# Performance work log

Hardware: AMD Instinct MI355X
Metric: run time of the kernel (lower is better)

## Reference

```python
import jax, jax.numpy as jnp
import numpy as np

B, C, H, W = 8, 512, 64, 64
IC = C // 2  # inter_channel


def setup_inputs() -> dict:
    key = jax.random.key(0)
    ks = jax.random.split(key, 10)
    s = 0.02
    return {
        "x": jax.random.normal(ks[0], (B, C, H, W), dtype=jnp.float32),
        "y": jax.random.normal(ks[1], (B, C, H, W), dtype=jnp.float32),
        "w_phi": jax.random.normal(ks[2], (IC, C), dtype=jnp.float32) * s,
        "b_phi": jnp.zeros((IC,), dtype=jnp.float32),
        "w_theta": jax.random.normal(ks[3], (IC, C), dtype=jnp.float32) * s,
        "b_theta": jnp.zeros((IC,), dtype=jnp.float32),
        "w_g": jax.random.normal(ks[4], (IC, C), dtype=jnp.float32) * s,
        "b_g": jnp.zeros((IC,), dtype=jnp.float32),
        "w_mask": jax.random.normal(ks[5], (C, IC), dtype=jnp.float32) * s,
        "b_mask": jnp.zeros((C,), dtype=jnp.float32),
    }


def _conv1x1(w, b, t):
    # t: [b, cin, h, w]; 1x1 conv == channel matmul
    return jnp.einsum('oc,bchw->bohw', w, t) + b[None, :, None, None]


def reference(x, y, w_phi, b_phi, w_theta, b_theta, w_g, b_g, w_mask, b_mask):
    b, c, h, w = x.shape
    ic = w_phi.shape[0]  # c // 2
    # Faithful to the torch code: conv outputs ic channels but is viewed as
    # (b, c, -1), so the sequence length is N = h*w//2 and feature dim is c.
    x_phi = _conv1x1(w_phi, b_phi, y).reshape(b, c, -1)              # [b, c, N]
    x_theta = _conv1x1(w_theta, b_theta, x).reshape(b, c, -1)
    x_theta = jnp.transpose(x_theta, (0, 2, 1))                      # [b, N, c]
    x_g = _conv1x1(w_g, b_g, x).reshape(b, c, -1)
    dict
    x_g = jnp.transpose(x_g, (0, 2, 1))                              # [b, N, c]
    scores = jnp.einsum('bnc,bcm->bnm', x_theta, x_phi)              # [b, N, N]
    attn = jax.nn.softmax(scores, axis=1)  # softmax over dim=1 (columns), as in torch
    out_nl = jnp.einsum('bnm,bmc->bnc', attn, x_g)                   # [b, N, c]
    out_nl = jnp.transpose(out_nl, (0, 2, 1)).reshape(b, ic, h, w)   # [b, ic, h, w]
    mask = _conv1x1(w_mask, b_mask, out_nl)                          # [b, c, h, w]
    return mask + x
```

## Files before the change

### kernel.cpp

```cpp
#include <hip/hip_runtime.h>
#include <hip/hip_bf16.h>


typedef __attribute__((ext_vector_type(8))) short short8;
typedef __attribute__((ext_vector_type(4))) short short4v;
typedef __attribute__((ext_vector_type(4))) float f32x4;

__device__ __forceinline__ short f2bf(float f) {
  union { __hip_bfloat16 h; short s; } u; u.h = __float2bfloat16(f); return u.s;
}
__device__ __forceinline__ float bf2f(short s) {
  union { short s; __hip_bfloat16 h; } u; u.s = s; return __bfloat162float(u.h);
}

__device__ __forceinline__ void async_ld16(const void* g, void* l) {
  __builtin_amdgcn_global_load_lds(
      (const __attribute__((address_space(1))) unsigned int*)(unsigned long long)g,
      (__attribute__((address_space(3))) unsigned int*)(unsigned int)(unsigned long long)l,
      16, 0, 0);
}

__device__ __forceinline__ short8 frag_sw(const short* Ds, int row, int q8)
{
  return *(const short8*)&Ds[row * 32 + (((q8 >> 3) ^ ((row >> 2) & 3)) << 3)];
}

__global__ __launch_bounds__(512, 4)
void ov_k(const short* __restrict__ Eg, const short* __restrict__ Gg,
          short* __restrict__ Cg)
{
  const int L = blockIdx.x;
  const int xcd = L & 7, k = L >> 3;
  const int slab = xcd + ((k >> 2) << 3);
  const int bz = slab >> 4, by = slab & 15, bx = k & 3;

  __shared__ __align__(16) short As[2][128 * 32];
  __shared__ __align__(16) short Bs[2][128 * 32];
  const short* A = Eg + ((long)bz << 22);
  const short* B = Gg + ((long)bz << 20);
  const int m0 = by * 128;
  const int n0 = bx * 128;
  const int t = threadIdx.x;
  const int wv = t >> 6, ln = t & 63;
  const int wr = wv >> 1, wc = wv & 1;
  const int fr = ln & 15, q8 = (ln >> 4) * 8;
  const int rowA = t >> 2;
  const int kcs = ((t & 3) ^ ((t >> 4) & 3)) * 8;

  f32x4 acc[2][4];
  #pragma unroll
  for (int i = 0; i < 2; i++)
    #pragma unroll
    for (int j = 0; j < 4; j++)
      #pragma unroll
      for (int r = 0; r < 4; r++) acc[i][j][r] = 0.f;

  async_ld16(A + (long)(m0 + rowA) * 2048 + kcs, &As[0][0] + wv * 512);
  async_ld16(B + (long)(n0 + rowA) * 2048 + kcs, &Bs[0][0] + wv * 512);
  __syncthreads();

  for (int kt = 1; kt < 64; kt++) {
    const int cur = (kt - 1) & 1, nxt = kt & 1;
    async_ld16(A + (long)(m0 + rowA) * 2048 + kt * 32 + kcs, &As[nxt][0] + wv * 512);
    async_ld16(B + (long)(n0 + rowA) * 2048 + kt * 32 + kcs, &Bs[nxt][0] + wv * 512);
    short8 af[2], bfr[4];
    #pragma unroll
    for (int mi = 0; mi < 2; mi++) af[mi] = frag_sw(&As[cur][0], wr * 32 + mi * 16 + fr, q8);
    #pragma unroll
    for (int ni = 0; ni < 4; ni++) bfr[ni] = frag_sw(&Bs[cur][0], wc * 64 + ni * 16 + fr, q8);
    #pragma unroll
    for (int mi = 0; mi < 2; mi++)
      #pragma unroll
      for (int ni = 0; ni < 4; ni++)
        acc[mi][ni] = __builtin_amdgcn_mfma_f32_16x16x32_bf16(af[mi], bfr[ni], acc[mi][ni], 0, 0, 0);
    __syncthreads();
  }
  {
    short8 af[2], bfr[4];
    #pragma unroll
    for (int mi = 0; mi < 2; mi++) af[mi] = frag_sw(&As[1][0], wr * 32 + mi * 16 + fr, q8);
    #pragma unroll
    for (int ni = 0; ni < 4; ni++) bfr[ni] = frag_sw(&Bs[1][0], wc * 64 + ni * 16 + fr, q8);
    #pragma unroll
    for (int mi = 0; mi < 2; mi++)
      #pragma unroll
      for (int ni = 0; ni < 4; ni++)
        acc[mi][ni] = __builtin_amdgcn_mfma_f32_16x16x32_bf16(af[mi], bfr[ni], acc[mi][ni], 0, 0, 0);
  }

  const int colb = n0 + wc * 64 + fr;
  const int rowb = m0 + wr * 32 + (ln >> 4) * 4;
  #pragma unroll
  for (int mi = 0; mi < 2; mi++)
    #pragma unroll
    for (int r = 0; r < 4; r++) {
      const int mr = rowb + mi * 16 + r;
      #pragma unroll
      for (int ni = 0; ni < 4; ni++)
        Cg[((long)bz << 20) + (long)mr * 512 + colb + ni * 16] = f2bf(acc[mi][ni][r]);
    }
}

__global__ __launch_bounds__(512, 2)
void conv_ptg(const float* __restrict__ x, const float* __restrict__ y,
              const short* __restrict__ wth, const short* __restrict__ wph,
              const short* __restrict__ wg,
              const float* __restrict__ bth, const float* __restrict__ bph,
              const float* __restrict__ bg,
              short* __restrict__ TPT2, short* __restrict__ G)
{
  __shared__ __align__(16) short As[2][128 * 32];
  __shared__ __align__(16) short Bs[2][256 * 32];
  __shared__ __align__(16) short Cs[2][256 * 32];
  const int slab = blockIdx.x;
  const bool isphi = slab >= 256;
  const bool doG = !isphi;
  const int s2 = slab & 255;
  const int img = s2 >> 5;
  const float* src = (isphi ? y : x) + (long)img * (512L * 4096);
  const int px0 = (s2 & 31) * 128;
  const long m0 = (long)slab * 128;
  const short* W = isphi ? wph : wth;
  const float* bias = isphi ? bph : bth;
  const int t = threadIdx.x;
  const int wv = t >> 6, ln = t & 63;
  const int wpx = wv >> 2, wic = wv & 3;
  const int fr = ln & 15, q8 = (ln >> 4) * 8;
  const int g4 = (t >> 5) * 4, p4 = (t & 31) * 4;
  const int w2 = wv - 4;
  const int kcs = ((ln & 3) ^ (ln >> 4)) * 8;

  f32x4 acc[4][4], accg[4][4];
  #pragma unroll
  for (int i = 0; i < 4; i++)
    #pragma unroll
    for (int j = 0; j < 4; j++)
      #pragma unroll
      for (int r = 0; r < 4; r++) { acc[i][j][r] = 0.f; accg[i][j][r] = 0.f; }

  if (t >= 256) {
    #pragma unroll
    for (int j = 0; j < 4; j++)
      async_ld16(W + (long)(w2 * 64 + j * 16 + (ln >> 2)) * 512 + kcs,
                 &Bs[0][(w2 * 64 + j * 16) * 32]);
    if (doG) {
      #pragma unroll
      for (int j = 0; j < 4; j++)
        async_ld16(wg + (long)(w2 * 64 + j * 16 + (ln >> 2)) * 512 + kcs,
                   &Cs[0][(w2 * 64 + j * 16) * 32]);
    }
  } else {
    f32x4 r[4];
    #pragma unroll
    for (int i = 0; i < 4; i++)
      r[i] = *(const f32x4*)&src[(long)(g4 + i) * 4096 + px0 + p4];
    #pragma unroll
    for (int j = 0; j < 4; j++) {
      short4v w;
      w[0] = f2bf(r[0][j]); w[1] = f2bf(r[1][j]); w[2] = f2bf(r[2][j]); w[3] = f2bf(r[3][j]);
      const int px = p4 + j;
      const int u = (g4 >> 3) ^ ((px >> 2) & 3);
      *(short4v*)&As[0][px * 32 + u * 8 + (g4 & 4)] = w;
    }
  }
  __syncthreads();

  for (int k = 1; k < 16; k++) {
    const int cur = (k - 1) & 1, nxt = k & 1;
    f32x4 r[4];
    if (t >= 256) {
      #pragma unroll
      for (int j = 0; j < 4; j++)
        async_ld16(W + (long)(w2 * 64 + j * 16 + (ln >> 2)) * 512 + k * 32 + kcs,
                   &Bs[nxt][(w2 * 64 + j * 16) * 32]);
      if (doG) {
        #pragma unroll
        for (int j = 0; j < 4; j++)
          async_ld16(wg + (long)(w2 * 64 + j * 16 + (ln >> 2)) * 512 + k * 32 + kcs,
                     &Cs[nxt][(w2 * 64 + j * 16) * 32]);
      }
    } else {
      #pragma unroll
      for (int i = 0; i < 4; i++)
        r[i] = *(const f32x4*)&src[(long)(k * 32 + g4 + i) * 4096 + px0 + p4];
    }
    short8 af[4], bfv[4];
    #pragma unroll
    for (int mi = 0; mi < 4; mi++) af[mi] = frag_sw(&As[cur][0], wpx * 64 + mi * 16 + fr, q8);
    #pragma unroll
    for (int ni = 0; ni < 4; ni++) bfv[ni] = frag_sw(&Bs[cur][0], wic * 64 + ni * 16 + fr, q8);
    #pragma unroll
    for (int mi = 0; mi < 4; mi++)
      #pragma unroll
      for (int ni = 0; ni < 4; ni++)
        acc[mi][ni] = __builtin_amdgcn_mfma_f32_16x16x32_bf16(af[mi], bfv[ni], acc[mi][ni], 0, 0, 0);
    if (doG) {
      short8 ag[4], bg2[4];
      #pragma unroll
      for (int mi = 0; mi < 4; mi++) ag[mi] = frag_sw(&Cs[cur][0], wic * 64 + mi * 16 + fr, q8);
      #pragma unroll
      for (int ni = 0; ni < 4; ni++) bg2[ni] = frag_sw(&As[cur][0], wpx * 64 + ni * 16 + fr, q8);
      #pragma unroll
      for (int mi = 0; mi < 4; mi++)
        #pragma unroll
        for (int ni = 0; ni < 4; ni++)
          accg[mi][ni] = __builtin_amdgcn_mfma_f32_16x16x32_bf16(ag[mi], bg2[ni], accg[mi][ni], 0, 0, 0);
    }
    if (t < 256) {
      #pragma unroll
      for (int j = 0; j < 4; j++) {
        short4v w;
        w[0] = f2bf(r[0][j]); w[1] = f2bf(r[1][j]); w[2] = f2bf(r[2][j]); w[3] = f2bf(r[3][j]);
        const int px = p4 + j;
        const int u = (g4 >> 3) ^ ((px >> 2) & 3);
        *(short4v*)&As[nxt][px * 32 + u * 8 + (g4 & 4)] = w;
      }
    }
    __syncthreads();
  }

  {
    short8 af[4], bfv[4];
    #pragma unroll
    for (int mi = 0; mi < 4; mi++) af[mi] = frag_sw(&As[1][0], wpx * 64 + mi * 16 + fr, q8);
    #pragma unroll
    for (int ni = 0; ni < 4; ni++) bfv[ni] = frag_sw(&Bs[1][0], wic * 64 + ni * 16 + fr, q8);
    #pragma unroll
    for (int mi = 0; mi < 4; mi++)
      #pragma unroll
      for (int ni = 0; ni < 4; ni++)
        acc[mi][ni] = __builtin_amdgcn_mfma_f32_16x16x32_bf16(af[mi], bfv[ni], acc[mi][ni], 0, 0, 0);
    if (doG) {
      short8 ag[4], bg2[4];
      #pragma unroll
      for (int mi = 0; mi < 4; mi++) ag[mi] = frag_sw(&Cs[1][0], wic * 64 + mi * 16 + fr, q8);
      #pragma unroll
      for (int ni = 0; ni < 4; ni++) bg2[ni] = frag_sw(&As[1][0], wpx * 64 + ni * 16 + fr, q8);
      #pragma unroll
      for (int mi = 0; mi < 4; mi++)
        #pragma unroll
        for (int ni = 0; ni < 4; ni++)
          accg[mi][ni] = __builtin_amdgcn_mfma_f32_16x16x32_bf16(ag[mi], bg2[ni], accg[mi][ni], 0, 0, 0);
    }
  }

  const int colic = wic * 64 + fr;
  float cb[4];
  #pragma unroll
  for (int ni = 0; ni < 4; ni++) cb[ni] = bias[colic + ni * 16];
  #pragma unroll
  for (int mi = 0; mi < 4; mi++)
    #pragma unroll
    for (int r = 0; r < 4; r++) {
      const long m = m0 + wpx * 64 + mi * 16 + (ln >> 4) * 4 + r;
      #pragma unroll
      for (int ni = 0; ni < 4; ni++)
        TPT2[m * 256 + colic + ni * 16] = f2bf(acc[mi][ni][r] + cb[ni]);
    }

  if (doG) {
    const int colpx = px0 + wpx * 64 + fr;
    #pragma unroll
    for (int mi = 0; mi < 4; mi++)
      #pragma unroll
      for (int r = 0; r < 4; r++) {
        const int ic = wic * 64 + mi * 16 + (ln >> 4) * 4 + r;
        const float badd = bg[ic];
        #pragma unroll
        for (int ni = 0; ni < 4; ni++)
          G[((long)img << 20) + (long)ic * 4096 + colpx + ni * 16] = f2bf(accg[mi][ni][r] + badd);
      }
  }
}

__global__ __launch_bounds__(256)
void scores_k(const short* __restrict__ TT2, const short* __restrict__ PT2,
              short* __restrict__ ST, float* __restrict__ pstats)
{
  __shared__ __align__(16) short As[2][128 * 32];
  __shared__ __align__(16) short Bs[2][128 * 32];
  const int bz = blockIdx.z, by = blockIdx.y, bx = blockIdx.x;
  const int t = threadIdx.x;
  const int wv = t >> 6, ln = t & 63;
  const int wm = (wv >> 1) * 64, wn = (wv & 1) * 64;
  const int fr = ln & 15, q8 = (ln >> 4) * 8;
  const int rowA = t >> 2;
  const int kcs = ((t & 3) ^ ((t >> 4) & 3)) * 8;

  const short* Abase = TT2 + ((long)(bz * 4096 + by * 128)) * 256;
  const short* Bbase = PT2 + ((long)(bz * 4096 + bx * 128)) * 256;

  f32x4 acc[4][4];
  #pragma unroll
  for (int i = 0; i < 4; i++)
    #pragma unroll
    for (int j = 0; j < 4; j++)
      #pragma unroll
      for (int r = 0; r < 4; r++) acc[i][j][r] = 0.f;

  #define SC_STAGE(s, buf)                                                     \
    {                                                                          \
      const long hoff = (long)((s) >> 3) * 2048 * 256;                         \
      const int kk = ((s) & 7) * 32;                                           \
      _Pragma("unroll")                                                        \
      for (int sv = 0; sv < 2; sv++) {                                         \
        async_ld16(Abase + hoff + (long)(sv * 64 + rowA) * 256 + kk + kcs,     \
                   &As[buf][0] + (sv * 256 + wv * 64) * 8);                    \
        async_ld16(Bbase + hoff + (long)(sv * 64 + rowA) * 256 + kk + kcs,     \
                   &Bs[buf][0] + (sv * 256 + wv * 64) * 8);                    \
      }                                                                        \
    }

  SC_STAGE(0, 0);
  __syncthreads();
  for (int s = 1; s < 16; s++) {
    const int cur = (s - 1) & 1, nxt = s & 1;
    SC_STAGE(s, nxt);
    short8 af[4], bfr[4];
    #pragma unroll
    for (int mi = 0; mi < 4; mi++) af[mi] = frag_sw(&As[cur][0], wm + mi * 16 + fr, q8);
    #pragma unroll
    for (int ni = 0; ni < 4; ni++) bfr[ni] = frag_sw(&Bs[cur][0], wn + ni * 16 + fr, q8);
    #pragma unroll
    for (int mi = 0; mi < 4; mi++)
      #pragma unroll
      for (int ni = 0; ni < 4; ni++)
        acc[mi][ni] = __builtin_amdgcn_mfma_f32_16x16x32_bf16(af[mi], bfr[ni], acc[mi][ni], 0, 0, 0);
    __syncthreads();
  }
  {
    short8 af[4], bfr[4];
    #pragma unroll
    for (int mi = 0; mi < 4; mi++) af[mi] = frag_sw(&As[1][0], wm + mi * 16 + fr, q8);
    #pragma unroll
    for (int ni = 0; ni < 4; ni++) bfr[ni] = frag_sw(&Bs[1][0], wn + ni * 16 + fr, q8);
    #pragma unroll
    for (int mi = 0; mi < 4; mi++)
      #pragma unroll
      for (int ni = 0; ni < 4; ni++)
        acc[mi][ni] = __builtin_amdgcn_mfma_f32_16x16x32_bf16(af[mi], bfr[ni], acc[mi][ni], 0, 0, 0);
  }
  #undef SC_STAGE

  const int colb = bx * 128 + wn + fr;
  const int rowb = by * 128 + wm + (ln >> 4) * 4;
  short* base = ST + ((long)bz << 22);
  float ps[4] = {0.f, 0.f, 0.f, 0.f};
  #pragma unroll
  for (int mi = 0; mi < 4; mi++)
    #pragma unroll
    for (int r = 0; r < 4; r++) {
      const long mr = rowb + mi * 16 + r;
      #pragma unroll
      for (int ni = 0; ni < 4; ni++) {
        float e = __expf(acc[mi][ni][r]);
        base[mr * 2048 + colb + ni * 16] = f2bf(e);
        ps[ni] += e;
      }
    }
  #pragma unroll
  for (int ni = 0; ni < 4; ni++) {
    ps[ni] += __shfl_xor(ps[ni], 16);
    ps[ni] += __shfl_xor(ps[ni], 32);
  }
  float* part = (float*)&As[0][0];
  if (ln < 16) {
    #pragma unroll
    for (int ni = 0; ni < 4; ni++)
      part[(wv >> 1) * 128 + wn + ni * 16 + fr] = ps[ni];
  }
  __syncthreads();
  if (t < 128)
    pstats[((long)(bz * 16 + by)) * 2048 + bx * 128 + t] = part[t] + part[128 + t];
}

__global__ __launch_bounds__(256)
void zfinal(const float* __restrict__ pstats, float* __restrict__ invZ)
{
  const int g = blockIdx.x * 256 + threadIdx.x;
  const int b = g >> 11, col = g & 2047;
  float S = 0.f;
  #pragma unroll
  for (int rc = 0; rc < 16; rc++) S += pstats[((long)(b * 16 + rc)) * 2048 + col];
  invZ[g] = 1.f / S;
}

__global__ __launch_bounds__(256)
void g_scale(short* __restrict__ G, const float* __restrict__ invZ)
{
  const long base = ((long)blockIdx.x * 256 + threadIdx.x) * 8;
  const int bz = (int)(base >> 20);
  const int n2 = (int)(base & 4095);
  const float* z = invZ + bz * 2048 + (n2 & 2047);
  short8 v = *(short8*)&G[base];
  f32x4 z0 = *(const f32x4*)z;
  f32x4 z1 = *(const f32x4*)(z + 4);
  #pragma unroll
  for (int j = 0; j < 4; j++) { v[j] = f2bf(bf2f(v[j]) * z0[j]); v[4 + j] = f2bf(bf2f(v[4 + j]) * z1[j]); }
  *(short8*)&G[base] = v;
}

__global__ __launch_bounds__(256)
void mask_k(const short* __restrict__ Wm20, const short* __restrict__ Wm21,
            const short* __restrict__ OVT, const float* __restrict__ bmask,
            const float* __restrict__ x, float* __restrict__ out)
{
  __shared__ __align__(16) short As[2][128 * 32];
  __shared__ __align__(16) short Bs[2][128 * 32];
  const int bz = blockIdx.z;
  const int n0 = blockIdx.x * 128;
  const int m0 = blockIdx.y * 128;
  const short* A = (n0 >= 2048) ? Wm21 : Wm20;
  const short* B = OVT + ((long)bz << 20) + (long)(n0 & 2047) * 512;
  const int t = threadIdx.x;
  const int wv = t >> 6, ln = t & 63;
  const int wm = (wv >> 1) * 64, wn = (wv & 1) * 64;
  const int fr = ln & 15, q8 = (ln >> 4) * 8;
  const int rowA = t >> 2;
  const int kcs = ((t & 3) ^ ((t >> 4) & 3)) * 8;

  f32x4 acc[4][4];
  #pragma unroll
  for (int i = 0; i < 4; i++)
    #pragma unroll
    for (int j = 0; j < 4; j++)
      #pragma unroll
      for (int r = 0; r < 4; r++) acc[i][j][r] = 0.f;

  #define MK_STAGE(s, buf)                                                     \
    {                                                                          \
      const int kk = (s) * 32;                                                 \
      _Pragma("unroll")                                                        \
      for (int sv = 0; sv < 2; sv++) {                                         \
        async_ld16(A + (long)(m0 + sv * 64 + rowA) * 512 + kk + kcs,           \
                   &As[buf][0] + (sv * 256 + wv * 64) * 8);                    \
        async_ld16(B + (long)(sv * 64 + rowA) * 512 + kk + kcs,                \
                   &Bs[buf][0] + (sv * 256 + wv * 64) * 8);                    \
      }                                                                        \
    }

  MK_STAGE(0, 0);
  __syncthreads();
  for (int s = 1; s < 16; s++) {
    const int cur = (s - 1) & 1, nxt = s & 1;
    MK_STAGE(s, nxt);
    short8 af[4], bfr[4];
    #pragma unroll
    for (int mi = 0; mi < 4; mi++) af[mi] = frag_sw(&As[cur][0], wm + mi * 16 + fr, q8);
    #pragma unroll
    for (int ni = 0; ni < 4; ni++) bfr[ni] = frag_sw(&Bs[cur][0], wn + ni * 16 + fr, q8);
    #pragma unroll
    for (int mi = 0; mi < 4; mi++)
      #pragma unroll
      for (int ni = 0; ni < 4; ni++)
        acc[mi][ni] = __builtin_amdgcn_mfma_f32_16x16x32_bf16(af[mi], bfr[ni], acc[mi][ni], 0, 0, 0);
    __syncthreads();
  }
  {
    short8 af[4], bfr[4];
    #pragma unroll
    for (int mi = 0; mi < 4; mi++) af[mi] = frag_sw(&As[1][0], wm + mi * 16 + fr, q8);
    #pragma unroll
    for (int ni = 0; ni < 4; ni++) bfr[ni] = frag_sw(&Bs[1][0], wn + ni * 16 + fr, q8);
    #pragma unroll
    for (int mi = 0; mi < 4; mi++)
      #pragma unroll
      for (int ni = 0; ni < 4; ni++)
        acc[mi][ni] = __builtin_amdgcn_mfma_f32_16x16x32_bf16(af[mi], bfr[ni], acc[mi][ni], 0, 0, 0);
  }
  #undef MK_STAGE

  const int colb = n0 + wn + fr;
  const int rowb = m0 + wm + (ln >> 4) * 4;
  #pragma unroll
  for (int mi = 0; mi < 4; mi++)
    #pragma unroll
    for (int r = 0; r < 4; r++) {
      const int mr = rowb + mi * 16 + r;
      const float badd = bmask[mr];
      const long rbase = ((long)bz * 512 + mr) * 4096;
      #pragma unroll
      for (int ni = 0; ni < 4; ni++) {
        const int cc = colb + ni * 16;
        out[rbase + cc] = acc[mi][ni][r] + badd + x[rbase + cc];
      }
    }
}

__global__ __launch_bounds__(256)
void wconv2(const float* w_phi, const float* w_theta, const float* w_g,
            const float* w_mask,
            short* wph, short* wth, short* wg, short* Wm20, short* Wm21)
{
  const int seg = blockIdx.x >> 6;
  const int blk = blockIdx.x & 63;
  const int i0 = blk * 2048 + threadIdx.x * 8;
  if (seg < 3) {
    const float* s = seg == 0 ? w_phi : seg == 1 ? w_theta : w_g;
    short* d = seg == 0 ? wph : seg == 1 ? wth : wg;
    f32x4 a = *(const f32x4*)&s[i0];
    f32x4 b = *(const f32x4*)&s[i0 + 4];
    short8 o;
    #pragma unroll
    for (int j = 0; j < 4; j++) { o[j] = f2bf(a[j]); o[4 + j] = f2bf(b[j]); }
    *(short8*)&d[i0] = o;
  } else {
    const int o = i0 >> 8;
    f32x4 a = *(const f32x4*)&w_mask[i0];
    f32x4 b = *(const f32x4*)&w_mask[i0 + 4];
    short v[8];
    #pragma unroll
    for (int j = 0; j < 4; j++) { v[j] = f2bf(a[j]); v[4 + j] = f2bf(b[j]); }
    short8 a0, a1, b0, b1;
    #pragma unroll
    for (int j = 0; j < 4; j++) {
      a0[2 * j] = v[j];     a0[2 * j + 1] = 0;
      a1[2 * j] = v[4 + j]; a1[2 * j + 1] = 0;
      b0[2 * j] = 0;        b0[2 * j + 1] = v[j];
      b1[2 * j] = 0;        b1[2 * j + 1] = v[4 + j];
    }
    const long base = (long)o * 512 + 2 * (i0 & 255);
    *(short8*)&Wm20[base] = a0; *(short8*)&Wm20[base + 8] = a1;
    *(short8*)&Wm21[base] = b0; *(short8*)&Wm21[base + 8] = b1;
  }
}

extern "C" void kernel_launch(void* const* d_in, const int* in_sizes, int n_in,
                              void* d_out, int out_size, void* d_ws, size_t ws_size,
                              hipStream_t stream)
{
  (void)in_sizes; (void)n_in; (void)out_size; (void)ws_size;
  const float* x       = (const float*)d_in[0];
  const float* y       = (const float*)d_in[1];
  const float* w_phi   = (const float*)d_in[2];
  const float* b_phi   = (const float*)d_in[3];
  const float* w_theta = (const float*)d_in[4];
  const float* b_theta = (const float*)d_in[5];
  const float* w_g     = (const float*)d_in[6];
  const float* b_g     = (const float*)d_in[7];
  const float* w_mask  = (const float*)d_in[8];
  const float* b_mask  = (const float*)d_in[9];
  float* out = (float*)d_out;

  char* ws = (char*)d_ws;
  const long MB = 1L << 20;
  short* wph  = (short*)(ws + 0);
  short* wth  = (short*)(ws + 256 * 1024);
  short* wg   = (short*)(ws + 512 * 1024);
  short* Wm20 = (short*)(ws + 768 * 1024);
  short* Wm21 = (short*)(ws + 1280 * 1024);
  short* TPT2 = (short*)(ws + 66 * MB);
  short* G    = (short*)(ws + 98 * MB);
  short* ST   = (short*)(ws + 2 * MB);
  float* pstats = (float*)(ws + 114 * MB);
  float* invZ   = (float*)(ws + 115 * MB);
  short* OVT  = (short*)(ws + 66 * MB);

  dim3 blk(256, 1, 1);
  dim3 blk8(512, 1, 1);

  wconv2<<<dim3(256, 1, 1), blk, 0, stream>>>(w_phi, w_theta, w_g, w_mask,
                                              wph, wth, wg, Wm20, Wm21);

  conv_ptg<<<dim3(512, 1, 1), blk8, 0, stream>>>(x, y, wth, wph, wg,
                                                 b_theta, b_phi, b_g, TPT2, G);

  scores_k<<<dim3(16, 16, 8), blk, 0, stream>>>(TPT2, TPT2 + 32768L * 256, ST, pstats);
  zfinal<<<dim3(64, 1, 1), blk, 0, stream>>>(pstats, invZ);
  g_scale<<<dim3(4096, 1, 1), blk, 0, stream>>>(G, invZ);

  ov_k<<<dim3(512, 1, 1), blk8, 0, stream>>>(ST, G, OVT);

  mask_k<<<dim3(32, 4, 8), blk, 0, stream>>>(Wm20, Wm21, OVT, b_mask, x, out);
}
```

Measured before the change: 372.3 us.

## Triple-buffer LDS in GEMM kernels with partial vmcnt waits

Converts the double-buffered async global-to-LDS pipelines in ov_k, scores_k and mask_k into three-stage pipelines. Each barrier now waits only until the previous stage's loads are done (vmcnt(N)), leaving one prefetch in flight. The goal is to hide global load latency behind MFMA work. LDS per block grows by half, which may limit occupancy, especially for ov_k with launch_bounds(512,4). The scores_k partial-stats scratch moves to buffer 1 to avoid clobbering data still in use.

```diff
diff --git a/kernel.cpp b/kernel.cpp
--- a/kernel.cpp
+++ b/kernel.cpp
@@ -20,6 +20,10 @@
       16, 0, 0);
 }
 
+#define CBAR(N)                                                                \
+  asm volatile("s_waitcnt vmcnt(" #N ") lgkmcnt(0)" ::: "memory");             \
+  __builtin_amdgcn_s_barrier();
+
 __device__ __forceinline__ short8 frag_sw(const short* Ds, int row, int q8)
 {
   return *(const short8*)&Ds[row * 32 + (((q8 >> 3) ^ ((row >> 2) & 3)) << 3)];
@@ -34,8 +38,8 @@
   const int slab = xcd + ((k >> 2) << 3);
   const int bz = slab >> 4, by = slab & 15, bx = k & 3;
 
-  __shared__ __align__(16) short As[2][128 * 32];
-  __shared__ __align__(16) short Bs[2][128 * 32];
+  __shared__ __align__(16) short As[3][128 * 32];
+  __shared__ __align__(16) short Bs[3][128 * 32];
   const short* A = Eg + ((long)bz << 22);
   const short* B = Gg + ((long)bz << 20);
   const int m0 = by * 128;
@@ -55,38 +59,48 @@
       #pragma unroll
       for (int r = 0; r < 4; r++) acc[i][j][r] = 0.f;
 
-  async_ld16(A + (long)(m0 + rowA) * 2048 + kcs, &As[0][0] + wv * 512);
-  async_ld16(B + (long)(n0 + rowA) * 2048 + kcs, &Bs[0][0] + wv * 512);
-  __syncthreads();
-
-  for (int kt = 1; kt < 64; kt++) {
-    const int cur = (kt - 1) & 1, nxt = kt & 1;
-    async_ld16(A + (long)(m0 + rowA) * 2048 + kt * 32 + kcs, &As[nxt][0] + wv * 512);
-    async_ld16(B + (long)(n0 + rowA) * 2048 + kt * 32 + kcs, &Bs[nxt][0] + wv * 512);
-    short8 af[2], bfr[4];
-    #pragma unroll
-    for (int mi = 0; mi < 2; mi++) af[mi] = frag_sw(&As[cur][0], wr * 32 + mi * 16 + fr, q8);
-    #pragma unroll
-    for (int ni = 0; ni < 4; ni++) bfr[ni] = frag_sw(&Bs[cur][0], wc * 64 + ni * 16 + fr, q8);
-    #pragma unroll
-    for (int mi = 0; mi < 2; mi++)
-      #pragma unroll
-      for (int ni = 0; ni < 4; ni++)
-        acc[mi][ni] = __builtin_amdgcn_mfma_f32_16x16x32_bf16(af[mi], bfr[ni], acc[mi][ni], 0, 0, 0);
-    __syncthreads();
-  }
-  {
-    short8 af[2], bfr[4];
-    #pragma unroll
-    for (int mi = 0; mi < 2; mi++) af[mi] = frag_sw(&As[1][0], wr * 32 + mi * 16 + fr, q8);
-    #pragma unroll
-    for (int ni = 0; ni < 4; ni++) bfr[ni] = frag_sw(&Bs[1][0], wc * 64 + ni * 16 + fr, q8);
-    #pragma unroll
-    for (int mi = 0; mi < 2; mi++)
-      #pragma unroll
-      for (int ni = 0; ni < 4; ni++)
-        acc[mi][ni] = __builtin_amdgcn_mfma_f32_16x16x32_bf16(af[mi], bfr[ni], acc[mi][ni], 0, 0, 0);
-  }
+  #define OV_STAGE(kt, buf)                                                    \
+    async_ld16(A + (long)(m0 + rowA) * 2048 + (kt) * 32 + kcs,                 \
+               &As[buf][0] + wv * 512);                                        \
+    async_ld16(B + (long)(n0 + rowA) * 2048 + (kt) * 32 + kcs,                 \
+               &Bs[buf][0] + wv * 512);
+
+  #define OV_COMPUTE(cbuf)                                                     \
+    {                                                                          \
+      const short* Ac = &As[cbuf][0];                                          \
+      const short* Bc = &Bs[cbuf][0];                                          \
+      short8 af[2], bfr[4];                                                    \
+      _Pragma("unroll")                                                        \
+      for (int mi = 0; mi < 2; mi++)                                           \
+        af[mi] = frag_sw(Ac, wr * 32 + mi * 16 + fr, q8);                      \
+      _Pragma("unroll")                                                        \
+      for (int ni = 0; ni < 4; ni++)                                           \
+        bfr[ni] = frag_sw(Bc, wc * 64 + ni * 16 + fr, q8);                     \
+      _Pragma("unroll")                                                        \
+      for (int mi = 0; mi < 2; mi++)                                           \
+        _Pragma("unroll")                                                      \
+        for (int ni = 0; ni < 4; ni++)                                         \
+          acc[mi][ni] = __builtin_amdgcn_mfma_f32_16x16x32_bf16(               \
+              af[mi], bfr[ni], acc[mi][ni], 0, 0, 0);                          \
+    }
+
+  OV_STAGE(0, 0);
+  OV_STAGE(1, 1);
+  CBAR(2)
+
+  int cs = 0, ss = 2;
+  for (int kt = 0; kt < 62; kt++) {
+    OV_STAGE(kt + 2, ss);
+    OV_COMPUTE(cs);
+    CBAR(2)
+    cs = (cs == 2) ? 0 : cs + 1;
+    ss = (ss == 2) ? 0 : ss + 1;
+  }
+  OV_COMPUTE(2)
+  CBAR(0)
+  OV_COMPUTE(0)
+  #undef OV_STAGE
+  #undef OV_COMPUTE
 
   const int colb = n0 + wc * 64 + fr;
   const int rowb = m0 + wr * 32 + (ln >> 4) * 4;
@@ -277,8 +291,8 @@
 void scores_k(const short* __restrict__ TT2, const short* __restrict__ PT2,
               short* __restrict__ ST, float* __restrict__ pstats)
 {
-  __shared__ __align__(16) short As[2][128 * 32];
-  __shared__ __align__(16) short Bs[2][128 * 32];
+  __shared__ __align__(16) short As[3][128 * 32];
+  __shared__ __align__(16) short Bs[3][128 * 32];
   const int bz = blockIdx.z, by = blockIdx.y, bx = blockIdx.x;
   const int t = threadIdx.x;
   const int wv = t >> 6, ln = t & 63;
@@ -311,36 +325,40 @@
       }                                                                        \
     }
 
+  #define SC_COMPUTE(cbuf)                                                     \
+    {                                                                          \
+      const short* Ac = &As[cbuf][0];                                          \
+      const short* Bc = &Bs[cbuf][0];                                          \
+      short8 af[4], bfr[4];                                                    \
+      _Pragma("unroll")                                                        \
+      for (int mi = 0; mi < 4; mi++) af[mi] = frag_sw(Ac, wm + mi * 16 + fr, q8); \
+      _Pragma("unroll")                                                        \
+      for (int ni = 0; ni < 4; ni++) bfr[ni] = frag_sw(Bc, wn + ni * 16 + fr, q8); \
+      _Pragma("unroll")                                                        \
+      for (int mi = 0; mi < 4; mi++)                                           \
+        _Pragma("unroll")                                                      \
+        for (int ni = 0; ni < 4; ni++)                                         \
+          acc[mi][ni] = __builtin_amdgcn_mfma_f32_16x16x32_bf16(               \
+              af[mi], bfr[ni], acc[mi][ni], 0, 0, 0);                          \
+    }
+
   SC_STAGE(0, 0);
-  __syncthreads();
-  for (int s = 1; s < 16; s++) {
-    const int cur = (s - 1) & 1, nxt = s & 1;
-    SC_STAGE(s, nxt);
-    short8 af[4], bfr[4];
-    #pragma unroll
-    for (int mi = 0; mi < 4; mi++) af[mi] = frag_sw(&As[cur][0], wm + mi * 16 + fr, q8);
-    #pragma unroll
-    for (int ni = 0; ni < 4; ni++) bfr[ni] = frag_sw(&Bs[cur][0], wn + ni * 16 + fr, q8);
-    #pragma unroll
-    for (int mi = 0; mi < 4; mi++)
-      #pragma unroll
-      for (int ni = 0; ni < 4; ni++)
-        acc[mi][ni] = __builtin_amdgcn_mfma_f32_16x16x32_bf16(af[mi], bfr[ni], acc[mi][ni], 0, 0, 0);
-    __syncthreads();
-  }
-  {
-    short8 af[4], bfr[4];
-    #pragma unroll
-    for (int mi = 0; mi < 4; mi++) af[mi] = frag_sw(&As[1][0], wm + mi * 16 + fr, q8);
-    #pragma unroll
-    for (int ni = 0; ni < 4; ni++) bfr[ni] = frag_sw(&Bs[1][0], wn + ni * 16 + fr, q8);
-    #pragma unroll
-    for (int mi = 0; mi < 4; mi++)
-      #pragma unroll
-      for (int ni = 0; ni < 4; ni++)
-        acc[mi][ni] = __builtin_amdgcn_mfma_f32_16x16x32_bf16(af[mi], bfr[ni], acc[mi][ni], 0, 0, 0);
-  }
+  SC_STAGE(1, 1);
+  CBAR(4)
+
+  int cs = 0, ss = 2;
+  for (int s = 0; s < 14; s++) {
+    SC_STAGE(s + 2, ss);
+    SC_COMPUTE(cs);
+    CBAR(4)
+    cs = (cs == 2) ? 0 : cs + 1;
+    ss = (ss == 2) ? 0 : ss + 1;
+  }
+  SC_COMPUTE(2)
+  CBAR(0)
+  SC_COMPUTE(0)
   #undef SC_STAGE
+  #undef SC_COMPUTE
 
   const int colb = bx * 128 + wn + fr;
   const int rowb = by * 128 + wm + (ln >> 4) * 4;
@@ -363,7 +381,7 @@
     ps[ni] += __shfl_xor(ps[ni], 16);
     ps[ni] += __shfl_xor(ps[ni], 32);
   }
-  float* part = (float*)&As[0][0];
+  float* part = (float*)&As[1][0];
   if (ln < 16) {
     #pragma unroll
     for (int ni = 0; ni < 4; ni++)
@@ -405,8 +423,8 @@
             const short* __restrict__ OVT, const float* __restrict__ bmask,
             const float* __restrict__ x, float* __restrict__ out)
 {
-  __shared__ __align__(16) short As[2][128 * 32];
-  __shared__ __align__(16) short Bs[2][128 * 32];
+  __shared__ __align__(16) short As[3][128 * 32];
+  __shared__ __align__(16) short Bs[3][128 * 32];
   const int bz = blockIdx.z;
   const int n0 = blockIdx.x * 128;
   const int m0 = blockIdx.y * 128;
@@ -439,36 +457,40 @@
       }                                                                        \
     }
 
+  #define MK_COMPUTE(cbuf)                                                     \
+    {                                                                          \
+      const short* Ac = &As[cbuf][0];                                          \
+      const short* Bc = &Bs[cbuf][0];                                          \
+      short8 af[4], bfr[4];                                                    \
+      _Pragma("unroll")                                                        \
+      for (int mi = 0; mi < 4; mi++) af[mi] = frag_sw(Ac, wm + mi * 16 + fr, q8); \
+      _Pragma("unroll")                                                        \
+      for (int ni = 0; ni < 4; ni++) bfr[ni] = frag_sw(Bc, wn + ni * 16 + fr, q8); \
+      _Pragma("unroll")                                                        \
+      for (int mi = 0; mi < 4; mi++)                                           \
+        _Pragma("unroll")                                                      \
+        for (int ni = 0; ni < 4; ni++)                                         \
+          acc[mi][ni] = __builtin_amdgcn_mfma_f32_16x16x32_bf16(               \
+              af[mi], bfr[ni], acc[mi][ni], 0, 0, 0);                          \
+    }
+
   MK_STAGE(0, 0);
-  __syncthreads();
-  for (int s = 1; s < 16; s++) {
-    const int cur = (s - 1) & 1, nxt = s & 1;
-    MK_STAGE(s, nxt);
-    short8 af[4], bfr[4];
-    #pragma unroll
-    for (int mi = 0; mi < 4; mi++) af[mi] = frag_sw(&As[cur][0], wm + mi * 16 + fr, q8);
-    #pragma unroll
-    for (int ni = 0; ni < 4; ni++) bfr[ni] = frag_sw(&Bs[cur][0], wn + ni * 16 + fr, q8);
-    #pragma unroll
-    for (int mi = 0; mi < 4; mi++)
-      #pragma unroll
-      for (int ni = 0; ni < 4; ni++)
-        acc[mi][ni] = __builtin_amdgcn_mfma_f32_16x16x32_bf16(af[mi], bfr[ni], acc[mi][ni], 0, 0, 0);
-    __syncthreads();
-  }
-  {
-    short8 af[4], bfr[4];
-    #pragma unroll
-    for (int mi = 0; mi < 4; mi++) af[mi] = frag_sw(&As[1][0], wm + mi * 16 + fr, q8);
-    #pragma unroll
-    for (int ni = 0; ni < 4; ni++) bfr[ni] = frag_sw(&Bs[1][0], wn + ni * 16 + fr, q8);
-    #pragma unroll
-    for (int mi = 0; mi < 4; mi++)
-      #pragma unroll
-      for (int ni = 0; ni < 4; ni++)
-        acc[mi][ni] = __builtin_amdgcn_mfma_f32_16x16x32_bf16(af[mi], bfr[ni], acc[mi][ni], 0, 0, 0);
-  }
+  MK_STAGE(1, 1);
+  CBAR(4)
+
+  int cs = 0, ss = 2;
+  for (int s = 0; s < 14; s++) {
+    MK_STAGE(s + 2, ss);
+    MK_COMPUTE(cs);
+    CBAR(4)
+    cs = (cs == 2) ? 0 : cs + 1;
+    ss = (ss == 2) ? 0 : ss + 1;
+  }
+  MK_COMPUTE(2)
+  CBAR(0)
+  MK_COMPUTE(0)
   #undef MK_STAGE
+  #undef MK_COMPUTE
 
   const int colb = n0 + wn + fr;
   const int rowb = m0 + wm + (ln >> 4) * 4;
```

Measured after the change: 357.4 us. 1.04x faster.
